# Performance work log

Measured on AMD Instinct MI355X. Metric: run time of the kernel, lower is better.

## Reference

```python
import jax, jax.numpy as jnp
import numpy as np


def setup_inputs() -> dict:
    key = jax.random.key(0)
    k1, k2, k3 = jax.random.split(key, 3)
    B, C_in, H, W = 32, 128, 64, 64
    C_out, KH, KW = 256, 3, 3
    x = jax.random.normal(k1, (B, C_in, H, W), dtype=jnp.float32)
    # kaiming_normal fan_out scale ~ sqrt(2 / (C_out*KH*KW)); plain normal is fine for a numeric reference
    weight = jax.random.normal(k2, (C_out, C_in, KH, KW), dtype=jnp.float32) * (2.0 / (C_out * KH * KW)) ** 0.5
    fan_in = C_in * KH * KW
    bound = 1.0 / (fan_in ** 0.5)
    bias = jax.random.uniform(k3, (C_out,), dtype=jnp.float32, minval=-bound, maxval=bound)
    return {"x": x, "weight": weight, "bias": bias}


def reference(x, weight, bias):
    # Equivalent of unfold (im2col) + matmul + fold with stride=1, padding=1:
    # a standard 2D convolution in NCHW/OIHW layout.
    out = jax.lax.conv_general_dilated(
        x, weight,
        window_strides=(1, 1),
        padding=((1, 1), (1, 1)),
        dimension_numbers=("NCHW", "OIHW", "NCHW"),
    )
    return out + bias[None, :, None, None]
```

## Files before the change

### kernel.cpp

```cpp
#include <hip/hip_runtime.h>

typedef __attribute__((ext_vector_type(4))) int   v4i;
typedef __attribute__((ext_vector_type(8))) short s8;
typedef __attribute__((ext_vector_type(4))) float f32x4;
typedef __attribute__((ext_vector_type(16))) float f32x16;

#define GLB __attribute__((address_space(1)))
#define LDS_AS __attribute__((address_space(3)))

__device__ __forceinline__ unsigned short f2bf(float f) {
  unsigned u = __builtin_bit_cast(unsigned, f);
  return (unsigned short)((u + 0x7fffu + ((u >> 16) & 1u)) >> 16);
}

__global__ void prep(const float* __restrict__ x, const float* __restrict__ w,
                     unsigned int* __restrict__ xw, unsigned short* __restrict__ ww) {
  int t = threadIdx.x;
  if (blockIdx.x >= 2048) {
    int o = (blockIdx.x - 2048) * 256 + t;
    int tap = o >> 15;
    int c   = (o >> 13) & 3;
    int cog = (o >> 10) & 7;
    int kk  = (o >> 9) & 1;
    int lh  = (o >> 8) & 1;
    int l31 = (o >> 3) & 31;
    int e   = o & 7;
    int co = cog * 32 + l31;
    int ci = c * 32 + kk * 16 + lh * 8 + e;
    ww[o] = f2bf(w[(co * 128 + ci) * 9 + tap]);
    return;
  }
  __shared__ float tile[128][65];
  int bid = blockIdx.x;
  int b = bid >> 6, h = bid & 63;
  {
    int wcol4 = (t & 15) * 4, cl = t >> 4;
    const float* src = x + ((size_t)(b * 128) * 64 + h) * 64 + wcol4;
#pragma unroll
    for (int j = 0; j < 8; ++j) {
      int ci = j * 16 + cl;
      f32x4 v = *(const f32x4*)(src + (size_t)ci * 4096);
      tile[ci][wcol4 + 0] = v[0];
      tile[ci][wcol4 + 1] = v[1];
      tile[ci][wcol4 + 2] = v[2];
      tile[ci][wcol4 + 3] = v[3];
    }
  }
  unsigned int* dst = xw + (size_t)((b * 66 + h + 1) * 66) * 64;
  if (t < 128) {
    int col = (t >> 6) ? 65 : 0;
    dst[(size_t)col * 64 + (t & 63)] = 0u;
  }
  if (h == 0 || h == 63) {
    unsigned int* rb = xw + (size_t)(b * 66 + (h == 0 ? 0 : 65)) * 66 * 64;
    for (int j = t; j < 66 * 64; j += 256) rb[j] = 0u;
  }
  __syncthreads();
  {
    int ci2 = (t & 63) * 2, wl = t >> 6;
#pragma unroll
    for (int j = 0; j < 16; ++j) {
      int wcol = j * 4 + wl;
      unsigned p = (unsigned)f2bf(tile[ci2][wcol]) |
                   ((unsigned)f2bf(tile[ci2 + 1][wcol]) << 16);
      dst[(size_t)(wcol + 1) * 64 + (t & 63)] = p;
    }
  }
}

__global__ __launch_bounds__(256, 3) void conv_mfma(
    const unsigned short* __restrict__ xw, const unsigned short* __restrict__ ww,
    const float* __restrict__ bias, float* __restrict__ out) {
  __shared__ unsigned short Xl[204 * 128];
  const int tid = threadIdx.x;
  const int lane = tid & 63;
  const int l31 = lane & 31, lh = lane >> 5;
  const int mw = tid >> 6;
  int bid = blockIdx.x;
  bid = (bid & 7) * 256 + (bid >> 3);
  const int b = bid >> 6, h0 = bid & 63;
  const unsigned xlb = (unsigned)(unsigned long long)((LDS_AS void*)Xl);

  {
    const char* xbase = (const char*)xw;
#pragma unroll
    for (int it = 0; it < 13; ++it) {
      int s = tid + it * 256;
      if (s < 3264) {
        int q = s >> 4, p = s & 15;
        int u = p ^ (q & 15);
        int rr = q / 68, cc = q - rr * 68;
        if (cc > 65) cc = 65;
        unsigned src = (unsigned)((b * 66 + h0 + rr) * 66 + cc) * 256u + (unsigned)u * 16u;
        __builtin_amdgcn_global_load_lds((const GLB unsigned int*)(xbase + src),
                                         (LDS_AS unsigned int*)&Xl[s * 8], 16, 0, 0);
      }
    }
  }

  f32x16 acc[2][2];
#pragma unroll
  for (int m = 0; m < 2; ++m)
#pragma unroll
    for (int n = 0; n < 2; ++n)
#pragma unroll
      for (int e = 0; e < 16; ++e) acc[m][n][e] = 0.f;

  v4i areg[3][4];
  v4i breg[2][4];
  const unsigned abyte = (unsigned)(mw * 4096 + lane * 16);

  #define ALOAD_ASM(slot, step)                                               \
    do {                                                                      \
      unsigned _wo = (unsigned)(step) * 16384u + abyte;                       \
      asm volatile("global_load_dwordx4 %0, %1, %2 offset:0"                  \
                   : "=v"(areg[slot][0]) : "v"(_wo), "s"(ww));                \
      asm volatile("global_load_dwordx4 %0, %1, %2 offset:1024"               \
                   : "=v"(areg[slot][1]) : "v"(_wo), "s"(ww));                \
      asm volatile("global_load_dwordx4 %0, %1, %2 offset:2048"               \
                   : "=v"(areg[slot][2]) : "v"(_wo), "s"(ww));                \
      asm volatile("global_load_dwordx4 %0, %1, %2 offset:3072"               \
                   : "=v"(areg[slot][3]) : "v"(_wo), "s"(ww));                \
    } while (0)

  #define BLOAD_ASM(slot, S)                                                  \
    do {                                                                      \
      const int _t = (S) >> 2, _c = (S) & 3;                                  \
      const int _kh = _t / 3, _kw = _t - _kh * 3;                             \
      const int _q0 = _kh * 68 + _kw + l31;                                   \
      const int _xq = (_q0 & 15) ^ lh;             \
      unsigned _a0 = xlb + (unsigned)((_q0 << 8) + (((_c * 4) ^ _xq) << 4));  \
      unsigned _a1 = xlb + (unsigned)((_q0 << 8) + (((_c * 4 + 2) ^ _xq) << 4)); \
      asm volatile("ds_read_b128 %0, %1" : "=v"(breg[slot][0]) : "v"(_a0));   \
      asm volatile("ds_read_b128 %0, %1 offset:8192"                          \
                   : "=v"(breg[slot][1]) : "v"(_a0));                         \
      asm volatile("ds_read_b128 %0, %1" : "=v"(breg[slot][2]) : "v"(_a1));   \
      asm volatile("ds_read_b128 %0, %1 offset:8192"                          \
                   : "=v"(breg[slot][3]) : "v"(_a1));                         \
    } while (0)

  #define KSTEP(S)                                                            \
    do {                                                                      \
      const int _s = (S);                                                     \
      if (_s < 34) ALOAD_ASM((_s + 2) % 3, _s + 2);                           \
      if (_s < 35) BLOAD_ASM((_s + 1) & 1, _s + 1);                           \
      if (_s < 34)                                                            \
        asm volatile("s_waitcnt vmcnt(8) lgkmcnt(4)" ::: "memory");           \
      else if (_s == 34)                                                      \
        asm volatile("s_waitcnt vmcnt(4) lgkmcnt(4)" ::: "memory");           \
      else                                                                    \
        asm volatile("s_waitcnt vmcnt(0) lgkmcnt(0)" ::: "memory");           \
      __builtin_amdgcn_sched_barrier(0);                                      \
      const int _cs = _s % 3, _bs = _s & 1;                                   \
      acc[0][0] = __builtin_amdgcn_mfma_f32_32x32x16_bf16(__builtin_bit_cast(s8, areg[_cs][0]), __builtin_bit_cast(s8, breg[_bs][0]), acc[0][0], 0, 0, 0); \
      acc[1][0] = __builtin_amdgcn_mfma_f32_32x32x16_bf16(__builtin_bit_cast(s8, areg[_cs][2]), __builtin_bit_cast(s8, breg[_bs][0]), acc[1][0], 0, 0, 0); \
      acc[0][1] = __builtin_amdgcn_mfma_f32_32x32x16_bf16(__builtin_bit_cast(s8, areg[_cs][0]), __builtin_bit_cast(s8, breg[_bs][1]), acc[0][1], 0, 0, 0); \
      acc[1][1] = __builtin_amdgcn_mfma_f32_32x32x16_bf16(__builtin_bit_cast(s8, areg[_cs][2]), __builtin_bit_cast(s8, breg[_bs][1]), acc[1][1], 0, 0, 0); \
      acc[0][0] = __builtin_amdgcn_mfma_f32_32x32x16_bf16(__builtin_bit_cast(s8, areg[_cs][1]), __builtin_bit_cast(s8, breg[_bs][2]), acc[0][0], 0, 0, 0); \
      acc[1][0] = __builtin_amdgcn_mfma_f32_32x32x16_bf16(__builtin_bit_cast(s8, areg[_cs][3]), __builtin_bit_cast(s8, breg[_bs][2]), acc[1][0], 0, 0, 0); \
      acc[0][1] = __builtin_amdgcn_mfma_f32_32x32x16_bf16(__builtin_bit_cast(s8, areg[_cs][1]), __builtin_bit_cast(s8, breg[_bs][3]), acc[0][1], 0, 0, 0); \
      acc[1][1] = __builtin_amdgcn_mfma_f32_32x32x16_bf16(__builtin_bit_cast(s8, areg[_cs][3]), __builtin_bit_cast(s8, breg[_bs][3]), acc[1][1], 0, 0, 0); \
    } while (0)

  ALOAD_ASM(0, 0);
  ALOAD_ASM(1, 1);
  asm volatile("s_waitcnt vmcnt(8)" ::: "memory");
  __builtin_amdgcn_sched_barrier(0);
  __builtin_amdgcn_s_barrier();
  BLOAD_ASM(0, 0);

#pragma unroll
  for (int s = 0; s < 36; ++s) KSTEP(s);

#pragma unroll
  for (int m = 0; m < 2; ++m)
#pragma unroll
    for (int rq = 0; rq < 4; ++rq) {
      const int cob = mw * 64 + m * 32 + 8 * rq + 4 * lh;
      const f32x4 bi = *(const f32x4*)(bias + cob);
#pragma unroll
      for (int n = 0; n < 2; ++n) {
        const int wc = n * 32 + l31;
        size_t base = ((size_t)(b * 256 + cob) * 64 + h0) * 64 + wc;
#pragma unroll
        for (int e = 0; e < 4; ++e)
          out[base + (size_t)e * 4096] = acc[m][n][rq * 4 + e] + bi[e];
      }
    }
}

__global__ void conv_naive(const float* __restrict__ x, const float* __restrict__ w,
                           const float* __restrict__ bias, float* __restrict__ out) {
  int i = blockIdx.x * 256 + threadIdx.x;
  int wc = i & 63, h = (i >> 6) & 63, co = (i >> 12) & 255, b = i >> 20;
  float s = bias[co];
  for (int ci = 0; ci < 128; ++ci)
#pragma unroll
    for (int kh = 0; kh < 3; ++kh) {
      int hh = h + kh - 1;
      if ((unsigned)hh >= 64u) continue;
#pragma unroll
      for (int kw = 0; kw < 3; ++kw) {
        int wg = wc + kw - 1;
        if ((unsigned)wg >= 64u) continue;
        s += x[((b * 128 + ci) * 64 + hh) * 64 + wg] *
             w[((co * 128 + ci) * 3 + kh) * 3 + kw];
      }
    }
  out[i] = s;
}

extern "C" void kernel_launch(void* const* d_in, const int* in_sizes, int n_in,
                              void* d_out, int out_size, void* d_ws, size_t ws_size,
                              hipStream_t stream) {
  const float* x    = (const float*)d_in[0];
  const float* w    = (const float*)d_in[1];
  const float* bias = (const float*)d_in[2];
  float* out = (float*)d_out;

  const size_t X_OFF  = 1ull << 20;
  const size_t XBYTES = 32ull * 66 * 66 * 128 * 2;
  const size_t NEED   = X_OFF + XBYTES;

  if (ws_size >= NEED) {
    unsigned short* ww = (unsigned short*)d_ws;
    unsigned short* xq = (unsigned short*)((char*)d_ws + X_OFF);
    hipLaunchKernelGGL(prep, dim3(3200), dim3(256), 0, stream, x, w,
                       (unsigned int*)xq, ww);
    hipLaunchKernelGGL(conv_mfma, dim3(2048), dim3(256), 0, stream, xq, ww, bias, out);
  } else {
    hipLaunchKernelGGL(conv_naive, dim3(131072), dim3(256), 0, stream, x, w, bias, out);
  }
}
```

Before: 93.44 us.

## Retile conv output block to 2 rows x 32 columns to shrink LDS halo

Each block now computes a 2-row by 32-column output tile instead of one full 64-wide row, so the staged input window becomes 4x34 pixels instead of 3x68. This cuts the LDS footprint from 204 to 136 pixel slots and the per-block global-to-LDS load volume, and the narrower width no longer needs the padding clamp. The cost is more halo overlap in the width direction and output stores of 32 contiguous floats per row instead of 64. The smaller LDS use could also allow more resident blocks.

```diff
diff --git a/kernel.cpp b/kernel.cpp
--- a/kernel.cpp
+++ b/kernel.cpp
@@ -71,27 +71,29 @@
 __global__ __launch_bounds__(256, 3) void conv_mfma(
     const unsigned short* __restrict__ xw, const unsigned short* __restrict__ ww,
     const float* __restrict__ bias, float* __restrict__ out) {
-  __shared__ unsigned short Xl[204 * 128];
+  __shared__ unsigned short Xl[136 * 128];
   const int tid = threadIdx.x;
   const int lane = tid & 63;
   const int l31 = lane & 31, lh = lane >> 5;
   const int mw = tid >> 6;
   int bid = blockIdx.x;
   bid = (bid & 7) * 256 + (bid >> 3);
-  const int b = bid >> 6, h0 = bid & 63;
+  const int b = bid >> 6;
+  const int hp = (bid >> 1) & 31, wsel = bid & 1;
+  const int h0 = hp << 1, w0 = wsel << 5;
   const unsigned xlb = (unsigned)(unsigned long long)((LDS_AS void*)Xl);
 
   {
     const char* xbase = (const char*)xw;
 #pragma unroll
-    for (int it = 0; it < 13; ++it) {
+    for (int it = 0; it < 9; ++it) {
       int s = tid + it * 256;
-      if (s < 3264) {
+      if (s < 2176) {
         int q = s >> 4, p = s & 15;
         int u = p ^ (q & 15);
-        int rr = q / 68, cc = q - rr * 68;
-        if (cc > 65) cc = 65;
-        unsigned src = (unsigned)((b * 66 + h0 + rr) * 66 + cc) * 256u + (unsigned)u * 16u;
+        int rr = q / 34, cc = q - rr * 34;
+        unsigned src = (unsigned)((b * 66 + h0 + rr) * 66 + (w0 + cc)) * 256u
+                       + (unsigned)u * 16u;
         __builtin_amdgcn_global_load_lds((const GLB unsigned int*)(xbase + src),
                                          (LDS_AS unsigned int*)&Xl[s * 8], 16, 0, 0);
       }
@@ -127,16 +129,17 @@
     do {                                                                      \
       const int _t = (S) >> 2, _c = (S) & 3;                                  \
       const int _kh = _t / 3, _kw = _t - _kh * 3;                             \
-      const int _q0 = _kh * 68 + _kw + l31;                                   \
-      const int _xq = (_q0 & 15) ^ lh;             \
-      unsigned _a0 = xlb + (unsigned)((_q0 << 8) + (((_c * 4) ^ _xq) << 4));  \
-      unsigned _a1 = xlb + (unsigned)((_q0 << 8) + (((_c * 4 + 2) ^ _xq) << 4)); \
-      asm volatile("ds_read_b128 %0, %1" : "=v"(breg[slot][0]) : "v"(_a0));   \
-      asm volatile("ds_read_b128 %0, %1 offset:8192"                          \
-                   : "=v"(breg[slot][1]) : "v"(_a0));                         \
-      asm volatile("ds_read_b128 %0, %1" : "=v"(breg[slot][2]) : "v"(_a1));   \
-      asm volatile("ds_read_b128 %0, %1 offset:8192"                          \
-                   : "=v"(breg[slot][3]) : "v"(_a1));                         \
+      const int _q0 = _kh * 34 + _kw + l31;                          \
+      const int _q1 = _q0 + 34;                                      \
+      const int _u0 = _c * 4, _u1 = _c * 4 + 2;                               \
+      unsigned _a00 = xlb + (unsigned)((_q0 << 8) + (((_u0 ^ (_q0 & 15)) ^ lh) << 4)); \
+      unsigned _a10 = xlb + (unsigned)((_q1 << 8) + (((_u0 ^ (_q1 & 15)) ^ lh) << 4)); \
+      unsigned _a01 = xlb + (unsigned)((_q0 << 8) + (((_u1 ^ (_q0 & 15)) ^ lh) << 4)); \
+      unsigned _a11 = xlb + (unsigned)((_q1 << 8) + (((_u1 ^ (_q1 & 15)) ^ lh) << 4)); \
+      asm volatile("ds_read_b128 %0, %1" : "=v"(breg[slot][0]) : "v"(_a00));  \
+      asm volatile("ds_read_b128 %0, %1" : "=v"(breg[slot][1]) : "v"(_a10));  \
+      asm volatile("ds_read_b128 %0, %1" : "=v"(breg[slot][2]) : "v"(_a01));  \
+      asm volatile("ds_read_b128 %0, %1" : "=v"(breg[slot][3]) : "v"(_a11));  \
     } while (0)
 
   #define KSTEP(S)                                                            \
@@ -180,8 +183,7 @@
       const f32x4 bi = *(const f32x4*)(bias + cob);
 #pragma unroll
       for (int n = 0; n < 2; ++n) {
-        const int wc = n * 32 + l31;
-        size_t base = ((size_t)(b * 256 + cob) * 64 + h0) * 64 + wc;
+        size_t base = ((size_t)(b * 256 + cob) * 64 + (h0 + n)) * 64 + w0 + l31;
 #pragma unroll
         for (int e = 0; e < 4; ++e)
           out[base + (size_t)e * 4096] = acc[m][n][rq * 4 + e] + bi[e];
```

New measurement: 104.3 us. 1.12x slower.
